# Kernel optimization log

Measured on AMD Instinct MI355X. Metric: run time of the kernel, lower is better.

The kernel has to match this reference:

```python
import jax, jax.numpy as jnp
import numpy as np

B, S, D, H = 4, 2048, 1024, 16
DEPTH = D // H
NEG = -1e9


def setup_inputs() -> dict:
    key = jax.random.key(0)
    ks = jax.random.split(key, 10)
    scale = 1.0 / np.sqrt(D)
    return {
        "query": jax.random.normal(ks[0], (B, S, D), jnp.float32),
        "key": jax.random.normal(ks[1], (B, S, D), jnp.float32),
        "value": jax.random.normal(ks[2], (B, S, D), jnp.float32),
        "mask": jnp.zeros((B, 1, 1, S), jnp.float32),
        "Wq": jax.random.normal(ks[3], (D, D), jnp.float32) * scale,
        "bq": jnp.zeros((D,), jnp.float32),
        "Wk": jax.random.normal(ks[4], (D, D), jnp.float32) * scale,
        "bk": jnp.zeros((D,), jnp.float32),
        "Wv": jax.random.normal(ks[5], (D, D), jnp.float32) * scale,
        "bv": jnp.zeros((D,), jnp.float32),
        "Wo": jax.random.normal(ks[6], (D, D), jnp.float32) * scale,
        "bo": jnp.zeros((D,), jnp.float32),
    }


def _split_heads(x):
    # [B, S, D] -> [B, H, S, depth]
    b, s, _ = x.shape
    return x.reshape(b, s, H, DEPTH).transpose(0, 2, 1, 3)


def reference(query, key, value, mask, Wq, bq, Wk, bk, Wv, bv, Wo, bo):
    q = _split_heads(query @ Wq + bq)
    k = _split_heads(key @ Wk + bk)
    v = _split_heads(value @ Wv + bv)
    # scaled dot-product attention
    logits = jnp.einsum("bhqd,bhkd->bhqk", q, k) / jnp.sqrt(
        jnp.asarray(DEPTH, jnp.float32))
    logits = logits + mask * NEG
    attn = jax.nn.softmax(logits, axis=-1)
    out = jnp.einsum("bhqk,bhkd->bhqd", attn, v)
    # merge heads: [B,H,S,depth] -> [B,S,D]
    out = out.transpose(0, 2, 1, 3).reshape(query.shape[0], -1, D)
    out = out @ Wo + bo
    return out, attn
```

## Files before the change

kernel.cpp:

```cpp
#include <hip/hip_runtime.h>
#include <stdint.h>


typedef float f32x4 __attribute__((ext_vector_type(4)));
typedef __bf16 bf16x8 __attribute__((ext_vector_type(8)));
typedef unsigned short u16x4 __attribute__((ext_vector_type(4)));
typedef unsigned short u16x8 __attribute__((ext_vector_type(8)));

#define LOG2E 1.44269504088896340736f

static __device__ __forceinline__ f32x4 mfma16(bf16x8 a, bf16x8 b, f32x4 c) {
  return __builtin_amdgcn_mfma_f32_16x16x32_bf16(a, b, c, 0, 0, 0);
}
static __device__ __forceinline__ unsigned short bfc(float f) {
  return __builtin_bit_cast(unsigned short, (__bf16)f);
}
static __device__ __forceinline__ float e2(float x) { return __builtin_amdgcn_exp2f(x); }

#define GLDS16(g, l)                                                    \
  __builtin_amdgcn_global_load_lds(                                     \
      (const __attribute__((address_space(1))) void*)(g),               \
      (__attribute__((address_space(3))) void*)(l), 16, 0, 0)

struct Ptr3 { const float* s[3]; unsigned short* d[3]; };
struct Ptr4 { const float* s[4]; unsigned short* d[4]; };
struct QKArgs {
  const unsigned short* A[2];
  const unsigned short* Bt[2];
  const float* bias[2];
  unsigned short* C[2];
};

__global__ void cvt3(Ptr3 p) {
  const int z = blockIdx.z;
  const int i = (blockIdx.x * 256 + threadIdx.x) * 4;
  f32x4 v = *(const f32x4*)(const void*)(p.s[z] + i);
  u16x4 o;
  o[0] = bfc(v[0]); o[1] = bfc(v[1]); o[2] = bfc(v[2]); o[3] = bfc(v[3]);
  *(u16x4*)(void*)(p.d[z] + i) = o;
}

__global__ void wtrans4(Ptr4 p) {
  __shared__ float t[32][33];
  const int z = blockIdx.z;
  const float* W = p.s[z];
  unsigned short* Wt = p.d[z];
  const int tx = threadIdx.x & 31, ty = threadIdx.x >> 5;
  const int n0 = blockIdx.x * 32, k0 = blockIdx.y * 32;
#pragma unroll
  for (int i = 0; i < 4; ++i)
    t[ty + i * 8][tx] = W[(size_t)(k0 + ty + i * 8) * 1024 + n0 + tx];
  __syncthreads();
#pragma unroll
  for (int i = 0; i < 4; ++i)
    Wt[(size_t)(n0 + ty + i * 8) * 1024 + k0 + tx] = bfc(t[tx][ty + i * 8]);
}

#define GEMM_PROLOG(Aptr, Btptr)                                        \
  __shared__ unsigned short sA[128 * 32];                               \
  __shared__ unsigned short sB[128 * 32];                               \
  const int tid = threadIdx.x;                                          \
  const int m0 = blockIdx.x << 7, n0 = blockIdx.y << 7;                 \
  const int w = tid >> 6, lane = tid & 63, g = lane >> 4, r = lane & 15;\
  const int wr = w >> 1, wc = w & 1;                                    \
  const int srow = tid >> 2;                                            \
  const int scol = (tid & 3) << 3;                                      \
  const unsigned short* ga = (Aptr) + (size_t)(m0 + srow) * 1024 + scol;\
  const unsigned short* gb = (Btptr) + (size_t)(n0 + srow) * 1024 + scol;\
  unsigned short* la = sA + tid * 8;                                    \
  unsigned short* lb = sB + tid * 8;

#define GEMM_KLOOP(SWAP)                                                \
  for (int kt = 0; kt < 32; ++kt) {                                     \
    const int ko = kt << 5;                                             \
    GLDS16(ga + ko, la);                                                \
    GLDS16(ga + ko + 64 * 1024, la + 64 * 32);                          \
    GLDS16(gb + ko, lb);                                                \
    GLDS16(gb + ko + 64 * 1024, lb + 64 * 32);                          \
    __syncthreads();                                                    \
    bf16x8 af[4], bfv[4];                                               \
    _Pragma("unroll")                                                   \
    for (int i = 0; i < 4; ++i) {                                       \
      af[i]  = *(const bf16x8*)(const void*)&sA[(wr * 64 + i * 16 + r) * 32 + g * 8]; \
      bfv[i] = *(const bf16x8*)(const void*)&sB[(wc * 64 + i * 16 + r) * 32 + g * 8]; \
    }                                                                   \
    _Pragma("unroll")                                                   \
    for (int i = 0; i < 4; ++i)                                         \
      _Pragma("unroll")                                                 \
      for (int j = 0; j < 4; ++j)                                       \
        acc[i][j] = (SWAP) ? mfma16(bfv[j], af[i], acc[i][j])           \
                           : mfma16(af[i], bfv[j], acc[i][j]);          \
    __syncthreads();                                                    \
  }

__global__ __launch_bounds__(256, 2) void gemm_qk(QKArgs args) {
  const int z = blockIdx.z;
  const f32x4 fz = {0.f, 0.f, 0.f, 0.f};
  f32x4 acc[4][4];
#pragma unroll
  for (int i = 0; i < 4; ++i)
#pragma unroll
    for (int j = 0; j < 4; ++j) acc[i][j] = fz;
  GEMM_PROLOG(args.A[z], args.Bt[z])
  GEMM_KLOOP(1)
  const float osc = (z == 0) ? (0.125f * LOG2E) : 1.0f;
  unsigned short* Cq = args.C[z];
  const float* bias = args.bias[z];
#pragma unroll
  for (int j = 0; j < 4; ++j) {
    const int nb = n0 + wc * 64 + j * 16 + g * 4;
    const f32x4 b4 = *(const f32x4*)(const void*)(bias + nb);
#pragma unroll
    for (int i = 0; i < 4; ++i) {
      const int m = m0 + wr * 64 + i * 16 + r;
      const int bb = m >> 11, s = m & 2047, hh = nb >> 6, d = nb & 63;
      u16x4 pk;
#pragma unroll
      for (int t = 0; t < 4; ++t) pk[t] = bfc((acc[i][j][t] + b4[t]) * osc);
      *(u16x4*)(void*)(Cq + (size_t)(bb * 16 + hh) * 131072 + (size_t)s * 64 + d) = pk;
    }
  }
}

__global__ __launch_bounds__(256, 2) void gemm_v(const unsigned short* __restrict__ A,
                                                 const unsigned short* __restrict__ Bt,
                                                 const float* __restrict__ bias,
                                                 unsigned short* __restrict__ C) {
  const f32x4 fz = {0.f, 0.f, 0.f, 0.f};
  f32x4 acc[4][4];
#pragma unroll
  for (int i = 0; i < 4; ++i)
#pragma unroll
    for (int j = 0; j < 4; ++j) acc[i][j] = fz;
  GEMM_PROLOG(A, Bt)
  GEMM_KLOOP(0)
#pragma unroll
  for (int j = 0; j < 4; ++j) {
    const int n = n0 + wc * 64 + j * 16 + r;
    const float bv = bias[n];
    const int hh = n >> 6, d = n & 63;
#pragma unroll
    for (int i = 0; i < 4; ++i) {
      const int m = m0 + wr * 64 + i * 16 + g * 4;
      const int bb = m >> 11, s = m & 2047;
      u16x4 pk;
#pragma unroll
      for (int t = 0; t < 4; ++t) pk[t] = bfc(acc[i][j][t] + bv);
      *(u16x4*)(void*)(C + (size_t)(bb * 16 + hh) * 131072 + (size_t)d * 2048 + s) = pk;
    }
  }
}

__global__ __launch_bounds__(256, 2) void gemm_o(const unsigned short* __restrict__ A,
                                                 const unsigned short* __restrict__ Bt,
                                                 const float* __restrict__ bias,
                                                 float* __restrict__ C) {
  const f32x4 fz = {0.f, 0.f, 0.f, 0.f};
  f32x4 acc[4][4];
#pragma unroll
  for (int i = 0; i < 4; ++i)
#pragma unroll
    for (int j = 0; j < 4; ++j) acc[i][j] = fz;
  GEMM_PROLOG(A, Bt)
  GEMM_KLOOP(1)
#pragma unroll
  for (int j = 0; j < 4; ++j) {
    const int nb = n0 + wc * 64 + j * 16 + g * 4;
    const f32x4 b4 = *(const f32x4*)(const void*)(bias + nb);
#pragma unroll
    for (int i = 0; i < 4; ++i) {
      const int m = m0 + wr * 64 + i * 16 + r;
      f32x4 c;
#pragma unroll
      for (int t = 0; t < 4; ++t) c[t] = acc[i][j][t] + b4[t];
      *(f32x4*)(void*)(C + (size_t)m * 1024 + nb) = c;
    }
  }
}

__global__ __launch_bounds__(256, 2) void attn_fused(const unsigned short* __restrict__ Qh,
                                                     const unsigned short* __restrict__ Kh,
                                                     const unsigned short* __restrict__ Vt,
                                                     const float* __restrict__ mask,
                                                     float* __restrict__ attn_out,
                                                     unsigned short* __restrict__ Obuf) {
  __shared__ unsigned short Plds[4][64 * 40];
  __shared__ float Osum[64][68];
  __shared__ float sml[4][64];

  const int blk = (blockIdx.x & 7) * 256 + (blockIdx.x >> 3);
  const int bh = blk >> 5;
  const int q0 = (blk & 31) << 6;
  const int b = bh >> 4, h = bh & 15;
  const int tid = threadIdx.x;
  const int w = tid >> 6, lane = tid & 63, g = lane >> 4, r = lane & 15;
  const float NEGM = -1e9f * LOG2E;

  const unsigned short* Qb = Qh + (size_t)bh * (2048 * 64);
  const unsigned short* Kb = Kh + (size_t)bh * (2048 * 64);
  const unsigned short* Vb = Vt + (size_t)bh * (64 * 2048);
  const float* mb = mask + (size_t)b * 2048;
  const f32x4 fz = {0.f, 0.f, 0.f, 0.f};

  bf16x8 qf[4][2];
#pragma unroll
  for (int qc = 0; qc < 4; ++qc)
#pragma unroll
    for (int hf = 0; hf < 2; ++hf)
      qf[qc][hf] = *(const bf16x8*)(const void*)(Qb + (size_t)(q0 + qc * 16 + r) * 64 + hf * 32 + g * 8);

  float lreg[4] = {0.f, 0.f, 0.f, 0.f};

  for (int step = 0; step < 16; ++step) {
    const int kk = (w << 9) + (step << 5);
    bf16x8 kf[2][2];
#pragma unroll
    for (int ks = 0; ks < 2; ++ks)
#pragma unroll
      for (int hf = 0; hf < 2; ++hf)
        kf[ks][hf] = *(const bf16x8*)(const void*)(Kb + (size_t)(kk + ks * 16 + r) * 64 + hf * 32 + g * 8);
    f32x4 mv0 = *(const f32x4*)(const void*)(mb + kk + g * 4);
    f32x4 mv1 = *(const f32x4*)(const void*)(mb + kk + 16 + g * 4);
    f32x4 mp0, mp1;
#pragma unroll
    for (int j = 0; j < 4; ++j) { mp0[j] = mv0[j] * NEGM; mp1[j] = mv1[j] * NEGM; }

#pragma unroll
    for (int qc = 0; qc < 4; ++qc) {
      f32x4 s0 = fz, s1 = fz;
      s0 = mfma16(kf[0][0], qf[qc][0], s0);
      s0 = mfma16(kf[0][1], qf[qc][1], s0);
      s1 = mfma16(kf[1][0], qf[qc][0], s1);
      s1 = mfma16(kf[1][1], qf[qc][1], s1);
      float p = 0.f;
#pragma unroll
      for (int j = 0; j < 4; ++j) p += e2(s0[j] + mp0[j]) + e2(s1[j] + mp1[j]);
      lreg[qc] += p;
    }
  }
#pragma unroll
  for (int qc = 0; qc < 4; ++qc) {
    lreg[qc] += __shfl_xor(lreg[qc], 16);
    lreg[qc] += __shfl_xor(lreg[qc], 32);
  }
  if (lane < 16) {
#pragma unroll
    for (int qc = 0; qc < 4; ++qc) sml[w][qc * 16 + lane] = lreg[qc];
  }
  __syncthreads();
  float cL[4];
#pragma unroll
  for (int qc = 0; qc < 4; ++qc) {
    const int q = qc * 16 + r;
    cL[qc] = -__log2f(sml[0][q] + sml[1][q] + sml[2][q] + sml[3][q]);
  }

  f32x4 oacc[4][4];
#pragma unroll
  for (int i = 0; i < 4; ++i)
#pragma unroll
    for (int j = 0; j < 4; ++j) oacc[i][j] = fz;

  float* ab = attn_out + (size_t)bh * 2048 * 2048;

  for (int step = 0; step < 16; ++step) {
    const int kk = (w << 9) + (step << 5);
    bf16x8 kf[2][2];
#pragma unroll
    for (int ks = 0; ks < 2; ++ks)
#pragma unroll
      for (int hf = 0; hf < 2; ++hf)
        kf[ks][hf] = *(const bf16x8*)(const void*)(Kb + (size_t)(kk + ks * 16 + r) * 64 + hf * 32 + g * 8);
    f32x4 mv0 = *(const f32x4*)(const void*)(mb + kk + g * 4);
    f32x4 mv1 = *(const f32x4*)(const void*)(mb + kk + 16 + g * 4);
    f32x4 mp[2];
#pragma unroll
    for (int j = 0; j < 4; ++j) { mp[0][j] = mv0[j] * NEGM; mp[1][j] = mv1[j] * NEGM; }

#pragma unroll
    for (int ks = 0; ks < 2; ++ks) {
#pragma unroll
      for (int qc = 0; qc < 4; ++qc) {
        f32x4 s = fz;
        s = mfma16(kf[ks][0], qf[qc][0], s);
        s = mfma16(kf[ks][1], qf[qc][1], s);
        f32x4 pv;
        u16x4 pb;
#pragma unroll
        for (int j = 0; j < 4; ++j) {
          const float val = e2(s[j] + mp[ks][j] + cL[qc]);
          pv[j] = val;
          pb[j] = bfc(val);
        }
        __builtin_nontemporal_store(
            pv, (f32x4*)(void*)(ab + (size_t)(q0 + qc * 16 + r) * 2048 + kk + ks * 16 + g * 4));
        *(u16x4*)(void*)(&Plds[w][(qc * 16 + r) * 40 + ks * 16 + g * 4]) = pb;
      }
    }
    bf16x8 vf[4];
#pragma unroll
    for (int dn = 0; dn < 4; ++dn)
      vf[dn] = *(const bf16x8*)(const void*)(Vb + (size_t)(dn * 16 + r) * 2048 + kk + g * 8);
#pragma unroll
    for (int qs = 0; qs < 4; ++qs) {
      const bf16x8 pa = *(const bf16x8*)(const void*)(&Plds[w][(qs * 16 + r) * 40 + g * 8]);
#pragma unroll
      for (int dn = 0; dn < 4; ++dn) oacc[qs][dn] = mfma16(pa, vf[dn], oacc[qs][dn]);
    }
  }

  for (int wv = 0; wv < 4; ++wv) {
    if (w == wv) {
#pragma unroll
      for (int qs = 0; qs < 4; ++qs)
#pragma unroll
        for (int dn = 0; dn < 4; ++dn)
#pragma unroll
          for (int j = 0; j < 4; ++j) {
            const int q = qs * 16 + g * 4 + j, d = dn * 16 + r;
            if (wv == 0) Osum[q][d] = oacc[qs][dn][j];
            else         Osum[q][d] += oacc[qs][dn][j];
          }
    }
    __syncthreads();
  }
  const int orow = tid >> 2, oc0 = (tid & 3) << 4;
#pragma unroll
  for (int half = 0; half < 2; ++half) {
    u16x8 pk;
#pragma unroll
    for (int j = 0; j < 8; ++j) pk[j] = bfc(Osum[orow][oc0 + half * 8 + j]);
    *(u16x8*)(void*)(Obuf + (size_t)(b * 2048 + q0 + orow) * 1024 + h * 64 + oc0 + half * 8) = pk;
  }
}

extern "C" void kernel_launch(void* const* d_in, const int* in_sizes, int n_in,
                              void* d_out, int out_size, void* d_ws, size_t ws_size,
                              hipStream_t stream) {
  const float* query = (const float*)d_in[0];
  const float* key_  = (const float*)d_in[1];
  const float* value = (const float*)d_in[2];
  const float* mask  = (const float*)d_in[3];
  const float* Wq = (const float*)d_in[4];
  const float* bq = (const float*)d_in[5];
  const float* Wk = (const float*)d_in[6];
  const float* bk = (const float*)d_in[7];
  const float* Wv = (const float*)d_in[8];
  const float* bv = (const float*)d_in[9];
  const float* Wo = (const float*)d_in[10];
  const float* bo = (const float*)d_in[11];

  uint8_t* ws = (uint8_t*)d_ws;
  unsigned short* XQ  = (unsigned short*)(ws);
  unsigned short* XK  = (unsigned short*)(ws + 16777216);
  unsigned short* XV  = (unsigned short*)(ws + 33554432);
  unsigned short* WTQ = (unsigned short*)(ws + 50331648);
  unsigned short* WTK = (unsigned short*)(ws + 52428800);
  unsigned short* WTV = (unsigned short*)(ws + 54525952);
  unsigned short* WTO = (unsigned short*)(ws + 56623104);
  unsigned short* QH  = (unsigned short*)(ws + 58720256);
  unsigned short* KH  = (unsigned short*)(ws + 75497472);
  unsigned short* VT  = (unsigned short*)(ws + 92274688);
  unsigned short* OB  = XQ;

  float* outp = (float*)d_out;
  float* attnp = outp + 8388608;

  Ptr3 pc = {{query, key_, value}, {XQ, XK, XV}};
  cvt3<<<dim3(8192, 1, 3), 256, 0, stream>>>(pc);
  Ptr4 pw = {{Wq, Wk, Wv, Wo}, {WTQ, WTK, WTV, WTO}};
  wtrans4<<<dim3(32, 32, 4), 256, 0, stream>>>(pw);
  QKArgs qk = {{XQ, XK}, {WTQ, WTK}, {bq, bk}, {QH, KH}};
  gemm_qk<<<dim3(64, 8, 2), 256, 0, stream>>>(qk);
  gemm_v<<<dim3(64, 8), 256, 0, stream>>>(XV, WTV, bv, VT);
  attn_fused<<<2048, 256, 0, stream>>>(QH, KH, VT, mask, attnp, OB);
  gemm_o<<<dim3(64, 8), 256, 0, stream>>>(OB, WTO, bo, outp);
}
```

Before: 507.0 us.

## Process four query tiles per block, fusing next tile's row-sum pass into current output pass

Each block now handles 256 query rows as four 64-row tiles instead of one. The row-sum (pass A) for the next tile is computed inside the same K loop as the probability and PV pass (pass B) of the current tile. This reuses each K fragment and mask load for both passes and cuts the separate pass-A K sweep for three of the four tiles. In exchange the grid shrinks from 2048 to 512 blocks and register pressure rises from holding two sets of Q fragments, which may lower occupancy or cause spills under launch_bounds(256,2).

```diff
diff --git a/kernel.cpp b/kernel.cpp
--- a/kernel.cpp
+++ b/kernel.cpp
@@ -178,6 +178,87 @@
   }
 }
 
+#define LOADQF(dst, qrow0)                                                        \
+  _Pragma("unroll")                                                               \
+  for (int qc = 0; qc < 4; ++qc)                                                  \
+    _Pragma("unroll")                                                             \
+    for (int hf = 0; hf < 2; ++hf)                                                \
+      dst[qc][hf] = *(const bf16x8*)(const void*)(Qb + (size_t)((qrow0) + qc * 16 + r) * 64 + hf * 32 + g * 8);
+
+#define LOADKF(kf, kk)                                                            \
+  _Pragma("unroll")                                                               \
+  for (int ks = 0; ks < 2; ++ks)                                                  \
+    _Pragma("unroll")                                                             \
+    for (int hf = 0; hf < 2; ++hf)                                                \
+      kf[ks][hf] = *(const bf16x8*)(const void*)(Kb + (size_t)((kk) + ks * 16 + r) * 64 + hf * 32 + g * 8);
+
+#define LOADMP(mp0, mp1, kk)                                                      \
+  {                                                                               \
+    f32x4 mv0 = *(const f32x4*)(const void*)(mb + (kk) + g * 4);                  \
+    f32x4 mv1 = *(const f32x4*)(const void*)(mb + (kk) + 16 + g * 4);             \
+    _Pragma("unroll")                                                             \
+    for (int j = 0; j < 4; ++j) { mp0[j] = mv0[j] * NEGM; mp1[j] = mv1[j] * NEGM; } \
+  }
+
+#define PASSA_CORE(qf, lreg, kf, mp0, mp1)                                        \
+  _Pragma("unroll")                                                               \
+  for (int qc = 0; qc < 4; ++qc) {                                                \
+    f32x4 s0 = fz, s1 = fz;                                                       \
+    s0 = mfma16(kf[0][0], qf[qc][0], s0);                                         \
+    s0 = mfma16(kf[0][1], qf[qc][1], s0);                                         \
+    s1 = mfma16(kf[1][0], qf[qc][0], s1);                                         \
+    s1 = mfma16(kf[1][1], qf[qc][1], s1);                                         \
+    float p = 0.f;                                                                \
+    _Pragma("unroll")                                                             \
+    for (int j = 0; j < 4; ++j) p += e2(s0[j] + mp0[j]) + e2(s1[j] + mp1[j]);     \
+    lreg[qc] += p;                                                                \
+  }
+
+#define PASSB_CORE(qf, cL, oacc, kf, mp0, mp1, qrow, kk)                          \
+  {                                                                               \
+    _Pragma("unroll")                                                             \
+    for (int ks = 0; ks < 2; ++ks) {                                              \
+      _Pragma("unroll")                                                           \
+      for (int qc = 0; qc < 4; ++qc) {                                            \
+        f32x4 s = fz;                                                             \
+        s = mfma16(kf[ks][0], qf[qc][0], s);                                      \
+        s = mfma16(kf[ks][1], qf[qc][1], s);                                      \
+        f32x4 pv;                                                                 \
+        u16x4 pb;                                                                 \
+        _Pragma("unroll")                                                         \
+        for (int j = 0; j < 4; ++j) {                                             \
+          const float val = e2(s[j] + (ks ? mp1[j] : mp0[j]) + cL[qc]);           \
+          pv[j] = val;                                                            \
+          pb[j] = bfc(val);                                                       \
+        }                                                                         \
+        __builtin_nontemporal_store(                                              \
+            pv, (f32x4*)(void*)(ab + (size_t)((qrow) + qc * 16 + r) * 2048 + (kk) + ks * 16 + g * 4)); \
+        *(u16x4*)(void*)(&Plds[w][(qc * 16 + r) * 40 + ks * 16 + g * 4]) = pb;    \
+      }                                                                           \
+    }                                                                             \
+    bf16x8 vf[4];                                                                 \
+    _Pragma("unroll")                                                             \
+    for (int dn = 0; dn < 4; ++dn)                                                \
+      vf[dn] = *(const bf16x8*)(const void*)(Vb + (size_t)(dn * 16 + r) * 2048 + (kk) + g * 8); \
+    _Pragma("unroll")                                                             \
+    for (int qs = 0; qs < 4; ++qs) {                                              \
+      const bf16x8 pa = *(const bf16x8*)(const void*)(&Plds[w][(qs * 16 + r) * 40 + g * 8]); \
+      _Pragma("unroll")                                                           \
+      for (int dn = 0; dn < 4; ++dn) oacc[qs][dn] = mfma16(pa, vf[dn], oacc[qs][dn]); \
+    }                                                                             \
+  }
+
+#define REDUCE_L(lreg)                                                            \
+  _Pragma("unroll")                                                               \
+  for (int qc = 0; qc < 4; ++qc) {                                                \
+    lreg[qc] += __shfl_xor(lreg[qc], 16);                                         \
+    lreg[qc] += __shfl_xor(lreg[qc], 32);                                         \
+  }                                                                               \
+  if (lane < 16) {                                                                \
+    _Pragma("unroll")                                                             \
+    for (int qc = 0; qc < 4; ++qc) sml[w][qc * 16 + lane] = lreg[qc];             \
+  }
+
 __global__ __launch_bounds__(256, 2) void attn_fused(const unsigned short* __restrict__ Qh,
                                                      const unsigned short* __restrict__ Kh,
                                                      const unsigned short* __restrict__ Vt,
@@ -188,9 +269,9 @@
   __shared__ float Osum[64][68];
   __shared__ float sml[4][64];
 
-  const int blk = (blockIdx.x & 7) * 256 + (blockIdx.x >> 3);
-  const int bh = blk >> 5;
-  const int q0 = (blk & 31) << 6;
+  const int blk = (blockIdx.x & 7) * 64 + (blockIdx.x >> 3);
+  const int bh = blk >> 3;
+  const int q0base = (blk & 7) << 8;
   const int b = bh >> 4, h = bh & 15;
   const int tid = threadIdx.x;
   const int w = tid >> 6, lane = tid & 63, g = lane >> 4, r = lane & 15;
@@ -201,136 +282,82 @@
   const unsigned short* Vb = Vt + (size_t)bh * (64 * 2048);
   const float* mb = mask + (size_t)b * 2048;
   const f32x4 fz = {0.f, 0.f, 0.f, 0.f};
-
-  bf16x8 qf[4][2];
-#pragma unroll
-  for (int qc = 0; qc < 4; ++qc)
-#pragma unroll
-    for (int hf = 0; hf < 2; ++hf)
-      qf[qc][hf] = *(const bf16x8*)(const void*)(Qb + (size_t)(q0 + qc * 16 + r) * 64 + hf * 32 + g * 8);
-
-  float lreg[4] = {0.f, 0.f, 0.f, 0.f};
-
-  for (int step = 0; step < 16; ++step) {
-    const int kk = (w << 9) + (step << 5);
-    bf16x8 kf[2][2];
-#pragma unroll
-    for (int ks = 0; ks < 2; ++ks)
-#pragma unroll
-      for (int hf = 0; hf < 2; ++hf)
-        kf[ks][hf] = *(const bf16x8*)(const void*)(Kb + (size_t)(kk + ks * 16 + r) * 64 + hf * 32 + g * 8);
-    f32x4 mv0 = *(const f32x4*)(const void*)(mb + kk + g * 4);
-    f32x4 mv1 = *(const f32x4*)(const void*)(mb + kk + 16 + g * 4);
-    f32x4 mp0, mp1;
-#pragma unroll
-    for (int j = 0; j < 4; ++j) { mp0[j] = mv0[j] * NEGM; mp1[j] = mv1[j] * NEGM; }
-
+  float* ab = attn_out + (size_t)bh * 2048 * 2048;
+
+  bf16x8 qfE[4][2], qfO[4][2];
+  LOADQF(qfE, q0base)
+
+  {
+    float lreg0[4] = {0.f, 0.f, 0.f, 0.f};
+    for (int step = 0; step < 16; ++step) {
+      const int kk = (w << 9) + (step << 5);
+      bf16x8 kf[2][2];
+      LOADKF(kf, kk)
+      f32x4 mp0, mp1;
+      LOADMP(mp0, mp1, kk)
+      PASSA_CORE(qfE, lreg0, kf, mp0, mp1)
+    }
+    REDUCE_L(lreg0)
+  }
+  __syncthreads();
+
+#pragma unroll
+  for (int t = 0; t < 4; ++t) {
+    bf16x8(&qa)[4][2] = (t & 1) ? qfO : qfE;
+    bf16x8(&qb)[4][2] = (t & 1) ? qfE : qfO;
+    const int qrow = q0base + t * 64;
+
+    float cL[4];
 #pragma unroll
     for (int qc = 0; qc < 4; ++qc) {
-      f32x4 s0 = fz, s1 = fz;
-      s0 = mfma16(kf[0][0], qf[qc][0], s0);
-      s0 = mfma16(kf[0][1], qf[qc][1], s0);
-      s1 = mfma16(kf[1][0], qf[qc][0], s1);
-      s1 = mfma16(kf[1][1], qf[qc][1], s1);
-      float p = 0.f;
-#pragma unroll
-      for (int j = 0; j < 4; ++j) p += e2(s0[j] + mp0[j]) + e2(s1[j] + mp1[j]);
-      lreg[qc] += p;
-    }
-  }
-#pragma unroll
-  for (int qc = 0; qc < 4; ++qc) {
-    lreg[qc] += __shfl_xor(lreg[qc], 16);
-    lreg[qc] += __shfl_xor(lreg[qc], 32);
-  }
-  if (lane < 16) {
-#pragma unroll
-    for (int qc = 0; qc < 4; ++qc) sml[w][qc * 16 + lane] = lreg[qc];
-  }
-  __syncthreads();
-  float cL[4];
-#pragma unroll
-  for (int qc = 0; qc < 4; ++qc) {
-    const int q = qc * 16 + r;
-    cL[qc] = -__log2f(sml[0][q] + sml[1][q] + sml[2][q] + sml[3][q]);
-  }
-
-  f32x4 oacc[4][4];
-#pragma unroll
-  for (int i = 0; i < 4; ++i)
-#pragma unroll
-    for (int j = 0; j < 4; ++j) oacc[i][j] = fz;
-
-  float* ab = attn_out + (size_t)bh * 2048 * 2048;
-
-  for (int step = 0; step < 16; ++step) {
-    const int kk = (w << 9) + (step << 5);
-    bf16x8 kf[2][2];
-#pragma unroll
-    for (int ks = 0; ks < 2; ++ks)
-#pragma unroll
-      for (int hf = 0; hf < 2; ++hf)
-        kf[ks][hf] = *(const bf16x8*)(const void*)(Kb + (size_t)(kk + ks * 16 + r) * 64 + hf * 32 + g * 8);
-    f32x4 mv0 = *(const f32x4*)(const void*)(mb + kk + g * 4);
-    f32x4 mv1 = *(const f32x4*)(const void*)(mb + kk + 16 + g * 4);
-    f32x4 mp[2];
-#pragma unroll
-    for (int j = 0; j < 4; ++j) { mp[0][j] = mv0[j] * NEGM; mp[1][j] = mv1[j] * NEGM; }
-
-#pragma unroll
-    for (int ks = 0; ks < 2; ++ks) {
-#pragma unroll
-      for (int qc = 0; qc < 4; ++qc) {
-        f32x4 s = fz;
-        s = mfma16(kf[ks][0], qf[qc][0], s);
-        s = mfma16(kf[ks][1], qf[qc][1], s);
-        f32x4 pv;
-        u16x4 pb;
-#pragma unroll
-        for (int j = 0; j < 4; ++j) {
-          const float val = e2(s[j] + mp[ks][j] + cL[qc]);
-          pv[j] = val;
-          pb[j] = bfc(val);
-        }
-        __builtin_nontemporal_store(
-            pv, (f32x4*)(void*)(ab + (size_t)(q0 + qc * 16 + r) * 2048 + kk + ks * 16 + g * 4));
-        *(u16x4*)(void*)(&Plds[w][(qc * 16 + r) * 40 + ks * 16 + g * 4]) = pb;
+      const int q = qc * 16 + r;
+      cL[qc] = -__log2f(sml[0][q] + sml[1][q] + sml[2][q] + sml[3][q]);
+    }
+
+    f32x4 oacc[4][4];
+#pragma unroll
+    for (int i = 0; i < 4; ++i)
+#pragma unroll
+      for (int j = 0; j < 4; ++j) oacc[i][j] = fz;
+
+    float lregB[4] = {0.f, 0.f, 0.f, 0.f};
+    if (t < 3) { LOADQF(qb, qrow + 64) }
+
+    for (int step = 0; step < 16; ++step) {
+      const int kk = (w << 9) + (step << 5);
+      bf16x8 kf[2][2];
+      LOADKF(kf, kk)
+      f32x4 mp0, mp1;
+      LOADMP(mp0, mp1, kk)
+      PASSB_CORE(qa, cL, oacc, kf, mp0, mp1, qrow, kk)
+      if (t < 3) { PASSA_CORE(qb, lregB, kf, mp0, mp1) }
+    }
+    if (t < 3) { REDUCE_L(lregB) }
+
+    for (int wv = 0; wv < 4; ++wv) {
+      if (w == wv) {
+#pragma unroll
+        for (int qs = 0; qs < 4; ++qs)
+#pragma unroll
+          for (int dn = 0; dn < 4; ++dn)
+#pragma unroll
+            for (int j = 0; j < 4; ++j) {
+              const int q = qs * 16 + g * 4 + j, d = dn * 16 + r;
+              if (wv == 0) Osum[q][d] = oacc[qs][dn][j];
+              else         Osum[q][d] += oacc[qs][dn][j];
+            }
       }
-    }
-    bf16x8 vf[4];
-#pragma unroll
-    for (int dn = 0; dn < 4; ++dn)
-      vf[dn] = *(const bf16x8*)(const void*)(Vb + (size_t)(dn * 16 + r) * 2048 + kk + g * 8);
-#pragma unroll
-    for (int qs = 0; qs < 4; ++qs) {
-      const bf16x8 pa = *(const bf16x8*)(const void*)(&Plds[w][(qs * 16 + r) * 40 + g * 8]);
-#pragma unroll
-      for (int dn = 0; dn < 4; ++dn) oacc[qs][dn] = mfma16(pa, vf[dn], oacc[qs][dn]);
-    }
-  }
-
-  for (int wv = 0; wv < 4; ++wv) {
-    if (w == wv) {
-#pragma unroll
-      for (int qs = 0; qs < 4; ++qs)
-#pragma unroll
-        for (int dn = 0; dn < 4; ++dn)
-#pragma unroll
-          for (int j = 0; j < 4; ++j) {
-            const int q = qs * 16 + g * 4 + j, d = dn * 16 + r;
-            if (wv == 0) Osum[q][d] = oacc[qs][dn][j];
-            else         Osum[q][d] += oacc[qs][dn][j];
-          }
+      __syncthreads();
+    }
+    const int orow = tid >> 2, oc0 = (tid & 3) << 4;
+#pragma unroll
+    for (int half = 0; half < 2; ++half) {
+      u16x8 pk;
+#pragma unroll
+      for (int j = 0; j < 8; ++j) pk[j] = bfc(Osum[orow][oc0 + half * 8 + j]);
+      *(u16x8*)(void*)(Obuf + (size_t)(b * 2048 + qrow + orow) * 1024 + h * 64 + oc0 + half * 8) = pk;
     }
     __syncthreads();
-  }
-  const int orow = tid >> 2, oc0 = (tid & 3) << 4;
-#pragma unroll
-  for (int half = 0; half < 2; ++half) {
-    u16x8 pk;
-#pragma unroll
-    for (int j = 0; j < 8; ++j) pk[j] = bfc(Osum[orow][oc0 + half * 8 + j]);
-    *(u16x8*)(void*)(Obuf + (size_t)(b * 2048 + q0 + orow) * 1024 + h * 64 + oc0 + half * 8) = pk;
   }
 }
 
@@ -373,6 +400,6 @@
   QKArgs qk = {{XQ, XK}, {WTQ, WTK}, {bq, bk}, {QH, KH}};
   gemm_qk<<<dim3(64, 8, 2), 256, 0, stream>>>(qk);
   gemm_v<<<dim3(64, 8), 256, 0, stream>>>(XV, WTV, bv, VT);
-  attn_fused<<<2048, 256, 0, stream>>>(QH, KH, VT, mask, attnp, OB);
+  attn_fused<<<512, 256, 0, stream>>>(QH, KH, VT, mask, attnp, OB);
   gemm_o<<<dim3(64, 8), 256, 0, stream>>>(OB, WTO, bo, outp);
 }
```

After: 491.1 us. 3.1% less time.

## Split fused attention into separate softmax-stats and PV kernels

Applied to the files above, without the earlier changes.

Splits the fused attention kernel in two. The first kernel computes only the per-row log-sum-exp normalisers and writes them to a workspace buffer, with a higher occupancy target. The second kernel reads those normalisers, writes the attention probabilities and does the PV product, with launch bounds raised from 2 to 3 blocks. The aim is better occupancy and register use in each phase, at the cost of an extra kernel launch, a small global round trip for the stats, and reloading Q in both kernels.

```diff
diff --git a/kernel.cpp b/kernel.cpp
--- a/kernel.cpp
+++ b/kernel.cpp
@@ -178,15 +178,95 @@
   }
 }
 
-__global__ __launch_bounds__(256, 2) void attn_fused(const unsigned short* __restrict__ Qh,
+
+#define LOADQF(dst, qrow0)                                                        \
+  _Pragma("unroll")                                                               \
+  for (int qc = 0; qc < 4; ++qc)                                                  \
+    _Pragma("unroll")                                                             \
+    for (int hf = 0; hf < 2; ++hf)                                                \
+      dst[qc][hf] = *(const bf16x8*)(const void*)(Qb + (size_t)((qrow0) + qc * 16 + r) * 64 + hf * 32 + g * 8);
+
+#define LOADKF(kf, kk)                                                            \
+  _Pragma("unroll")                                                               \
+  for (int ks = 0; ks < 2; ++ks)                                                  \
+    _Pragma("unroll")                                                             \
+    for (int hf = 0; hf < 2; ++hf)                                                \
+      kf[ks][hf] = *(const bf16x8*)(const void*)(Kb + (size_t)((kk) + ks * 16 + r) * 64 + hf * 32 + g * 8);
+
+#define LOADMP(mp0, mp1, kk)                                                      \
+  {                                                                               \
+    f32x4 mv0 = *(const f32x4*)(const void*)(mb + (kk) + g * 4);                  \
+    f32x4 mv1 = *(const f32x4*)(const void*)(mb + (kk) + 16 + g * 4);             \
+    _Pragma("unroll")                                                             \
+    for (int j = 0; j < 4; ++j) { mp0[j] = mv0[j] * NEGM; mp1[j] = mv1[j] * NEGM; } \
+  }
+
+__global__ __launch_bounds__(256, 4) void attn_stats(const unsigned short* __restrict__ Qh,
                                                      const unsigned short* __restrict__ Kh,
-                                                     const unsigned short* __restrict__ Vt,
                                                      const float* __restrict__ mask,
-                                                     float* __restrict__ attn_out,
-                                                     unsigned short* __restrict__ Obuf) {
+                                                     float* __restrict__ Ls) {
+  __shared__ float sml[4][64];
+  const int blk = (blockIdx.x & 7) * 256 + (blockIdx.x >> 3);
+  const int bh = blk >> 5;
+  const int q0 = (blk & 31) << 6;
+  const int b = bh >> 4;
+  const int tid = threadIdx.x;
+  const int w = tid >> 6, lane = tid & 63, g = lane >> 4, r = lane & 15;
+  const float NEGM = -1e9f * LOG2E;
+
+  const unsigned short* Qb = Qh + (size_t)bh * (2048 * 64);
+  const unsigned short* Kb = Kh + (size_t)bh * (2048 * 64);
+  const float* mb = mask + (size_t)b * 2048;
+  const f32x4 fz = {0.f, 0.f, 0.f, 0.f};
+
+  bf16x8 qf[4][2];
+  LOADQF(qf, q0)
+  float lreg[4] = {0.f, 0.f, 0.f, 0.f};
+
+  for (int step = 0; step < 16; ++step) {
+    const int kk = (w << 9) + (step << 5);
+    bf16x8 kf[2][2];
+    LOADKF(kf, kk)
+    f32x4 mp0, mp1;
+    LOADMP(mp0, mp1, kk)
+#pragma unroll
+    for (int qc = 0; qc < 4; ++qc) {
+      f32x4 s0 = fz, s1 = fz;
+      s0 = mfma16(kf[0][0], qf[qc][0], s0);
+      s0 = mfma16(kf[0][1], qf[qc][1], s0);
+      s1 = mfma16(kf[1][0], qf[qc][0], s1);
+      s1 = mfma16(kf[1][1], qf[qc][1], s1);
+      float p = 0.f;
+#pragma unroll
+      for (int j = 0; j < 4; ++j) p += e2(s0[j] + mp0[j]) + e2(s1[j] + mp1[j]);
+      lreg[qc] += p;
+    }
+  }
+#pragma unroll
+  for (int qc = 0; qc < 4; ++qc) {
+    lreg[qc] += __shfl_xor(lreg[qc], 16);
+    lreg[qc] += __shfl_xor(lreg[qc], 32);
+  }
+  if (lane < 16) {
+#pragma unroll
+    for (int qc = 0; qc < 4; ++qc) sml[w][qc * 16 + lane] = lreg[qc];
+  }
+  __syncthreads();
+  if (tid < 64) {
+    const float L = sml[0][tid] + sml[1][tid] + sml[2][tid] + sml[3][tid];
+    Ls[(size_t)bh * 2048 + q0 + tid] = -__log2f(L);
+  }
+}
+
+__global__ __launch_bounds__(256, 3) void attn_pv(const unsigned short* __restrict__ Qh,
+                                                  const unsigned short* __restrict__ Kh,
+                                                  const unsigned short* __restrict__ Vt,
+                                                  const float* __restrict__ mask,
+                                                  const float* __restrict__ Ls,
+                                                  float* __restrict__ attn_out,
+                                                  unsigned short* __restrict__ Obuf) {
   __shared__ unsigned short Plds[4][64 * 40];
   __shared__ float Osum[64][68];
-  __shared__ float sml[4][64];
 
   const int blk = (blockIdx.x & 7) * 256 + (blockIdx.x >> 3);
   const int bh = blk >> 5;
@@ -201,81 +281,27 @@
   const unsigned short* Vb = Vt + (size_t)bh * (64 * 2048);
   const float* mb = mask + (size_t)b * 2048;
   const f32x4 fz = {0.f, 0.f, 0.f, 0.f};
+  float* ab = attn_out + (size_t)bh * 2048 * 2048;
 
   bf16x8 qf[4][2];
+  LOADQF(qf, q0)
+  float cL[4];
 #pragma unroll
   for (int qc = 0; qc < 4; ++qc)
-#pragma unroll
-    for (int hf = 0; hf < 2; ++hf)
-      qf[qc][hf] = *(const bf16x8*)(const void*)(Qb + (size_t)(q0 + qc * 16 + r) * 64 + hf * 32 + g * 8);
-
-  float lreg[4] = {0.f, 0.f, 0.f, 0.f};
+    cL[qc] = Ls[(size_t)bh * 2048 + q0 + qc * 16 + r];
+
+  f32x4 oacc[4][4];
+#pragma unroll
+  for (int i = 0; i < 4; ++i)
+#pragma unroll
+    for (int j = 0; j < 4; ++j) oacc[i][j] = fz;
 
   for (int step = 0; step < 16; ++step) {
     const int kk = (w << 9) + (step << 5);
     bf16x8 kf[2][2];
-#pragma unroll
-    for (int ks = 0; ks < 2; ++ks)
-#pragma unroll
-      for (int hf = 0; hf < 2; ++hf)
-        kf[ks][hf] = *(const bf16x8*)(const void*)(Kb + (size_t)(kk + ks * 16 + r) * 64 + hf * 32 + g * 8);
-    f32x4 mv0 = *(const f32x4*)(const void*)(mb + kk + g * 4);
-    f32x4 mv1 = *(const f32x4*)(const void*)(mb + kk + 16 + g * 4);
+    LOADKF(kf, kk)
     f32x4 mp0, mp1;
-#pragma unroll
-    for (int j = 0; j < 4; ++j) { mp0[j] = mv0[j] * NEGM; mp1[j] = mv1[j] * NEGM; }
-
-#pragma unroll
-    for (int qc = 0; qc < 4; ++qc) {
-      f32x4 s0 = fz, s1 = fz;
-      s0 = mfma16(kf[0][0], qf[qc][0], s0);
-      s0 = mfma16(kf[0][1], qf[qc][1], s0);
-      s1 = mfma16(kf[1][0], qf[qc][0], s1);
-      s1 = mfma16(kf[1][1], qf[qc][1], s1);
-      float p = 0.f;
-#pragma unroll
-      for (int j = 0; j < 4; ++j) p += e2(s0[j] + mp0[j]) + e2(s1[j] + mp1[j]);
-      lreg[qc] += p;
-    }
-  }
-#pragma unroll
-  for (int qc = 0; qc < 4; ++qc) {
-    lreg[qc] += __shfl_xor(lreg[qc], 16);
-    lreg[qc] += __shfl_xor(lreg[qc], 32);
-  }
-  if (lane < 16) {
-#pragma unroll
-    for (int qc = 0; qc < 4; ++qc) sml[w][qc * 16 + lane] = lreg[qc];
-  }
-  __syncthreads();
-  float cL[4];
-#pragma unroll
-  for (int qc = 0; qc < 4; ++qc) {
-    const int q = qc * 16 + r;
-    cL[qc] = -__log2f(sml[0][q] + sml[1][q] + sml[2][q] + sml[3][q]);
-  }
-
-  f32x4 oacc[4][4];
-#pragma unroll
-  for (int i = 0; i < 4; ++i)
-#pragma unroll
-    for (int j = 0; j < 4; ++j) oacc[i][j] = fz;
-
-  float* ab = attn_out + (size_t)bh * 2048 * 2048;
-
-  for (int step = 0; step < 16; ++step) {
-    const int kk = (w << 9) + (step << 5);
-    bf16x8 kf[2][2];
-#pragma unroll
-    for (int ks = 0; ks < 2; ++ks)
-#pragma unroll
-      for (int hf = 0; hf < 2; ++hf)
-        kf[ks][hf] = *(const bf16x8*)(const void*)(Kb + (size_t)(kk + ks * 16 + r) * 64 + hf * 32 + g * 8);
-    f32x4 mv0 = *(const f32x4*)(const void*)(mb + kk + g * 4);
-    f32x4 mv1 = *(const f32x4*)(const void*)(mb + kk + 16 + g * 4);
-    f32x4 mp[2];
-#pragma unroll
-    for (int j = 0; j < 4; ++j) { mp[0][j] = mv0[j] * NEGM; mp[1][j] = mv1[j] * NEGM; }
+    LOADMP(mp0, mp1, kk)
 
 #pragma unroll
     for (int ks = 0; ks < 2; ++ks) {
@@ -288,7 +314,7 @@
         u16x4 pb;
 #pragma unroll
         for (int j = 0; j < 4; ++j) {
-          const float val = e2(s[j] + mp[ks][j] + cL[qc]);
+          const float val = e2(s[j] + (ks ? mp1[j] : mp0[j]) + cL[qc]);
           pv[j] = val;
           pb[j] = bfc(val);
         }
@@ -361,6 +387,7 @@
   unsigned short* QH  = (unsigned short*)(ws + 58720256);
   unsigned short* KH  = (unsigned short*)(ws + 75497472);
   unsigned short* VT  = (unsigned short*)(ws + 92274688);
+  float*          LS  = (float*)(ws + 109051904);
   unsigned short* OB  = XQ;
 
   float* outp = (float*)d_out;
@@ -373,6 +400,7 @@
   QKArgs qk = {{XQ, XK}, {WTQ, WTK}, {bq, bk}, {QH, KH}};
   gemm_qk<<<dim3(64, 8, 2), 256, 0, stream>>>(qk);
   gemm_v<<<dim3(64, 8), 256, 0, stream>>>(XV, WTV, bv, VT);
-  attn_fused<<<2048, 256, 0, stream>>>(QH, KH, VT, mask, attnp, OB);
+  attn_stats<<<2048, 256, 0, stream>>>(QH, KH, mask, LS);
+  attn_pv<<<2048, 256, 0, stream>>>(QH, KH, VT, mask, LS, attnp, OB);
   gemm_o<<<dim3(64, 8), 256, 0, stream>>>(OB, WTO, bo, outp);
 }
```

Measured after the change: 557.0 us. 9.9% more time.

## Stage softmax probabilities in LDS and write attention rows coalesced

Applied to the files above, without the earlier changes.

The attention-probability tile is now held in a larger per-wave LDS buffer (bf16) covering 128 keys. After each group of four key steps, the full rows are written to global memory as contiguous fp32 rows instead of scattered 16-byte stores from the MFMA layout. This targets the write efficiency of the large attention output. In exchange, the stored attention values are bf16-rounded before widening to fp32, which lowers their precision. LDS usage grows, and the old Osum array now aliases the staging buffer.

```diff
diff --git a/kernel.cpp b/kernel.cpp
--- a/kernel.cpp
+++ b/kernel.cpp
@@ -6,6 +6,7 @@
 typedef __bf16 bf16x8 __attribute__((ext_vector_type(8)));
 typedef unsigned short u16x4 __attribute__((ext_vector_type(4)));
 typedef unsigned short u16x8 __attribute__((ext_vector_type(8)));
+typedef unsigned int u32x2 __attribute__((ext_vector_type(2)));
 
 #define LOG2E 1.44269504088896340736f
 
@@ -16,6 +17,9 @@
   return __builtin_bit_cast(unsigned short, (__bf16)f);
 }
 static __device__ __forceinline__ float e2(float x) { return __builtin_amdgcn_exp2f(x); }
+static __device__ __forceinline__ float fb(unsigned int u) {
+  return __builtin_bit_cast(float, u);
+}
 
 #define GLDS16(g, l)                                                    \
   __builtin_amdgcn_global_load_lds(                                     \
@@ -184,8 +188,8 @@
                                                      const float* __restrict__ mask,
                                                      float* __restrict__ attn_out,
                                                      unsigned short* __restrict__ Obuf) {
-  __shared__ unsigned short Plds[4][64 * 40];
-  __shared__ float Osum[64][68];
+  constexpr int PITCH = 138;
+  __shared__ __align__(16) unsigned short PldsAll[4][64 * PITCH];
   __shared__ float sml[4][64];
 
   const int blk = (blockIdx.x & 7) * 256 + (blockIdx.x >> 3);
@@ -262,53 +266,67 @@
     for (int j = 0; j < 4; ++j) oacc[i][j] = fz;
 
   float* ab = attn_out + (size_t)bh * 2048 * 2048;
-
-  for (int step = 0; step < 16; ++step) {
-    const int kk = (w << 9) + (step << 5);
-    bf16x8 kf[2][2];
-#pragma unroll
-    for (int ks = 0; ks < 2; ++ks)
-#pragma unroll
-      for (int hf = 0; hf < 2; ++hf)
-        kf[ks][hf] = *(const bf16x8*)(const void*)(Kb + (size_t)(kk + ks * 16 + r) * 64 + hf * 32 + g * 8);
-    f32x4 mv0 = *(const f32x4*)(const void*)(mb + kk + g * 4);
-    f32x4 mv1 = *(const f32x4*)(const void*)(mb + kk + 16 + g * 4);
-    f32x4 mp[2];
-#pragma unroll
-    for (int j = 0; j < 4; ++j) { mp[0][j] = mv0[j] * NEGM; mp[1][j] = mv1[j] * NEGM; }
-
-#pragma unroll
-    for (int ks = 0; ks < 2; ++ks) {
-#pragma unroll
-      for (int qc = 0; qc < 4; ++qc) {
-        f32x4 s = fz;
-        s = mfma16(kf[ks][0], qf[qc][0], s);
-        s = mfma16(kf[ks][1], qf[qc][1], s);
-        f32x4 pv;
-        u16x4 pb;
-#pragma unroll
-        for (int j = 0; j < 4; ++j) {
-          const float val = e2(s[j] + mp[ks][j] + cL[qc]);
-          pv[j] = val;
-          pb[j] = bfc(val);
+  unsigned short* Pw = &PldsAll[w][0];
+  const int half = lane >> 5;
+  const int l5 = lane & 31;
+
+  for (int batch = 0; batch < 4; ++batch) {
+#pragma unroll
+    for (int sub = 0; sub < 4; ++sub) {
+      const int step = batch * 4 + sub;
+      const int kk = (w << 9) + (step << 5);
+      bf16x8 kf[2][2];
+#pragma unroll
+      for (int ks = 0; ks < 2; ++ks)
+#pragma unroll
+        for (int hf = 0; hf < 2; ++hf)
+          kf[ks][hf] = *(const bf16x8*)(const void*)(Kb + (size_t)(kk + ks * 16 + r) * 64 + hf * 32 + g * 8);
+      f32x4 mv0 = *(const f32x4*)(const void*)(mb + kk + g * 4);
+      f32x4 mv1 = *(const f32x4*)(const void*)(mb + kk + 16 + g * 4);
+      f32x4 mp[2];
+#pragma unroll
+      for (int j = 0; j < 4; ++j) { mp[0][j] = mv0[j] * NEGM; mp[1][j] = mv1[j] * NEGM; }
+
+#pragma unroll
+      for (int ks = 0; ks < 2; ++ks) {
+#pragma unroll
+        for (int qc = 0; qc < 4; ++qc) {
+          f32x4 s = fz;
+          s = mfma16(kf[ks][0], qf[qc][0], s);
+          s = mfma16(kf[ks][1], qf[qc][1], s);
+          u16x4 pb;
+#pragma unroll
+          for (int j = 0; j < 4; ++j) pb[j] = bfc(e2(s[j] + mp[ks][j] + cL[qc]));
+          *(u16x4*)(void*)(&Pw[(qc * 16 + r) * PITCH + sub * 32 + ks * 16 + g * 4]) = pb;
         }
-        __builtin_nontemporal_store(
-            pv, (f32x4*)(void*)(ab + (size_t)(q0 + qc * 16 + r) * 2048 + kk + ks * 16 + g * 4));
-        *(u16x4*)(void*)(&Plds[w][(qc * 16 + r) * 40 + ks * 16 + g * 4]) = pb;
       }
-    }
-    bf16x8 vf[4];
-#pragma unroll
-    for (int dn = 0; dn < 4; ++dn)
-      vf[dn] = *(const bf16x8*)(const void*)(Vb + (size_t)(dn * 16 + r) * 2048 + kk + g * 8);
-#pragma unroll
-    for (int qs = 0; qs < 4; ++qs) {
-      const bf16x8 pa = *(const bf16x8*)(const void*)(&Plds[w][(qs * 16 + r) * 40 + g * 8]);
-#pragma unroll
-      for (int dn = 0; dn < 4; ++dn) oacc[qs][dn] = mfma16(pa, vf[dn], oacc[qs][dn]);
-    }
-  }
-
+      bf16x8 vf[4];
+#pragma unroll
+      for (int dn = 0; dn < 4; ++dn)
+        vf[dn] = *(const bf16x8*)(const void*)(Vb + (size_t)(dn * 16 + r) * 2048 + kk + g * 8);
+#pragma unroll
+      for (int qs = 0; qs < 4; ++qs) {
+        const bf16x8 pa = *(const bf16x8*)(const void*)(&Pw[(qs * 16 + r) * PITCH + sub * 32 + g * 8]);
+#pragma unroll
+        for (int dn = 0; dn < 4; ++dn) oacc[qs][dn] = mfma16(pa, vf[dn], oacc[qs][dn]);
+      }
+    }
+    const int colb = (w << 9) + (batch << 7);
+#pragma unroll 4
+    for (int i = 0; i < 32; ++i) {
+      const int row = i * 2 + half;
+      const u32x2 u = *(const u32x2*)(const void*)(&Pw[row * PITCH + l5 * 4]);
+      f32x4 o;
+      o[0] = fb(u[0] << 16);
+      o[1] = fb(u[0] & 0xFFFF0000u);
+      o[2] = fb(u[1] << 16);
+      o[3] = fb(u[1] & 0xFFFF0000u);
+      __builtin_nontemporal_store(
+          o, (f32x4*)(void*)(ab + (size_t)(q0 + row) * 2048 + colb + l5 * 4));
+    }
+  }
+
+  float (*Osum)[68] = reinterpret_cast<float (*)[68]>(&PldsAll[0][0]);
   for (int wv = 0; wv < 4; ++wv) {
     if (w == wv) {
 #pragma unroll
@@ -326,11 +344,11 @@
   }
   const int orow = tid >> 2, oc0 = (tid & 3) << 4;
 #pragma unroll
-  for (int half = 0; half < 2; ++half) {
+  for (int hf2 = 0; hf2 < 2; ++hf2) {
     u16x8 pk;
 #pragma unroll
-    for (int j = 0; j < 8; ++j) pk[j] = bfc(Osum[orow][oc0 + half * 8 + j]);
-    *(u16x8*)(void*)(Obuf + (size_t)(b * 2048 + q0 + orow) * 1024 + h * 64 + oc0 + half * 8) = pk;
+    for (int j = 0; j < 8; ++j) pk[j] = bfc(Osum[orow][oc0 + hf2 * 8 + j]);
+    *(u16x8*)(void*)(Obuf + (size_t)(b * 2048 + q0 + orow) * 1024 + h * 64 + oc0 + hf2 * 8) = pk;
   }
 }
 
```

Result: faster. 449.3 us, median of 2 (-11.4%).
